# Performance work log

Hardware: AMD Instinct MI355X
Metric: run time of the kernel (lower is better)

## Reference

```python
import jax, jax.numpy as jnp
from jax import lax
import numpy as np

B, CIN, L = 16, 512, 1024
COUT, K = 1024, 5          # conv out channels (GLU halves to 512), kernel size
DW = 512                    # word_feat == attn_channels == img_conv channels
HW = 196                    # 14*14 image feature locations


def setup_inputs() -> dict:
    key = jax.random.key(0)
    ks = jax.random.split(key, 8)
    s = 0.02
    return {
        "x": jax.random.normal(ks[0], (B, CIN, L), jnp.float32),
        "word_embed": jax.random.normal(ks[1], (B, L, DW), jnp.float32),
        "img_conv": jax.random.normal(ks[2], (B, DW, 14, 14), jnp.float32),
        "prev_attn": jnp.zeros((B, L, HW), jnp.float32),  # passed through, unused
        "conv_v": jax.random.normal(ks[3], (COUT, CIN, K), jnp.float32) * s,
        "conv_g": jnp.ones((COUT,), jnp.float32),
        "conv_b": jnp.zeros((COUT,), jnp.float32),
        "fc1_w": jax.random.normal(ks[4], (DW, DW), jnp.float32) * s,
        "fc1_b": jnp.zeros((DW,), jnp.float32),
        "fc2_w": jax.random.normal(ks[5], (DW, DW), jnp.float32) * s,
        "fc2_b": jnp.zeros((DW,), jnp.float32),
    }


def reference(x, word_embed, img_conv, prev_attn,
              conv_v, conv_g, conv_b, fc1_w, fc1_b, fc2_w, fc2_b):
    k = conv_v.shape[-1]
    # weight norm (PyTorch default dim=0): w = g * v / ||v||_{(in,k)}
    v_norm = jnp.sqrt(jnp.sum(conv_v * conv_v, axis=(1, 2), keepdims=True))
    w = (conv_g[:, None, None] / v_norm) * conv_v
    # Conv1d, padding=k-1 on both sides -> length L + k - 1 after ConvS2S trim
    y = lax.conv_general_dilated(x, w, window_strides=(1,),
                                 padding=[(k - 1, k - 1)],
                                 dimension_numbers=("NCH", "OIH", "NCH"))
    y = y + conv_b[None, :, None]
    # dropout is identity in eval mode
    a, b = jnp.split(y, 2, axis=1)          # GLU over channel dim
    h = a * jax.nn.sigmoid(b)
    h = h[:, :, : -(k - 1)]                  # [B, DW, L]
    identity_attn = h
    # attn_fc1 on [B, L, DW] then add word embeddings
    q = jnp.einsum("bcl,ac->bla", h, fc1_w) + fc1_b + word_embed  # [B, L, DW]
    feat = img_conv.reshape(img_conv.shape[0], img_conv.shape[1], -1)  # [B, DW, HW]
    score = jnp.einsum("bla,bap->blp", q, feat)   # [B, L, HW]
    attn = jax.nn.softmax(score, axis=-1)         # softmax over image locations
    ctx = jnp.einsum("blp,bap->bla", attn, feat)  # [B, L, DW]
    o = jnp.einsum("bla,ca->blc", ctx, fc2_w) + fc2_b
    out = o.transpose(0, 2, 1) + identity_attn
    # identity.shape == out.shape (input_feat == output_feat/2) -> no downsample
    out = out + x
    return (out, word_embed, img_conv, attn)
```

## Files before the change

kernel.cpp:

```cpp
#include <hip/hip_runtime.h>
#include <math.h>

#define NB   16
#define NCIN 512
#define NL   1024
#define NCOUT 1024
#define NK   5
#define NDW  512
#define NHW  196
#define NP   208
#define NPK  224
#define NLG  1028

typedef unsigned short ushort_t;
typedef unsigned int uint_t;
typedef __attribute__((ext_vector_type(8))) short bf16x8;
typedef __attribute__((ext_vector_type(4))) float f32x4;

static __device__ __forceinline__ ushort_t f2bf(float f) {
  uint_t u = __builtin_bit_cast(uint_t, f);
  u += 0x7fff + ((u >> 16) & 1);
  return (ushort_t)(u >> 16);
}
static __device__ __forceinline__ float bf2f(ushort_t u) {
  uint_t v = ((uint_t)u) << 16;
  return __builtin_bit_cast(float, v);
}

#define BARM()    asm volatile("s_barrier" ::: "memory")
#define WAITVM8() asm volatile("s_waitcnt vmcnt(8)" ::: "memory")
#define WAITVM0() asm volatile("s_waitcnt vmcnt(0)" ::: "memory")

static __device__ __forceinline__ void gld16(const ushort_t* g, ushort_t* l) {
  __builtin_amdgcn_global_load_lds(
      (const __attribute__((address_space(1))) unsigned int*)g,
      (__attribute__((address_space(3))) unsigned int*)l, 16, 0, 0);
}

__global__ __launch_bounds__(256) void wnorm_kernel(
    const float* __restrict__ v, const float* __restrict__ g,
    ushort_t* __restrict__ wperm) {
  const int o = blockIdx.x;
  const float* vr = v + (size_t)o * (NCIN * NK);
  float s = 0.f;
  for (int j = threadIdx.x; j < NCIN * NK; j += 256) {
    float t = vr[j];
    s += t * t;
  }
  for (int off = 32; off; off >>= 1) s += __shfl_down(s, off, 64);
  __shared__ float red[4];
  __shared__ float scale_s;
  const int wid = threadIdx.x >> 6;
  if ((threadIdx.x & 63) == 0) red[wid] = s;
  __syncthreads();
  if (threadIdx.x == 0) {
    float tot = red[0] + red[1] + red[2] + red[3];
    scale_s = g[o] / sqrtf(tot);
  }
  __syncthreads();
  const float scale = scale_s;
  const int isB = (o >= NDW) ? 1 : 0;
  const int c = o - isB * NDW;
  const int j = (c >> 5) * 64 + isB * 32 + (c & 31);
#pragma unroll
  for (int dk = 0; dk < NK; ++dk) {
    for (int ci = threadIdx.x; ci < NCIN; ci += 256) {
      wperm[((size_t)dk * NCOUT + j) * NCIN + ci] = f2bf(vr[ci * NK + dk] * scale);
    }
  }
}

__global__ __launch_bounds__(256) void xpose_kernel(
    const float* __restrict__ x, ushort_t* __restrict__ xT) {
  const int b = blockIdx.z;
  const int ci0 = blockIdx.y * 64;
  const int l0 = blockIdx.x * 64;
  const int tid = threadIdx.x;
  __shared__ float t[64][65];
  const float* xb = x + ((size_t)b * NCIN + ci0) * NL + l0;
#pragma unroll
  for (int r = 0; r < 4; ++r) {
    int row = r * 16 + (tid >> 4);
    int col = (tid & 15) * 4;
    float4 v = *(const float4*)&xb[(size_t)row * NL + col];
    t[row][col + 0] = v.x; t[row][col + 1] = v.y;
    t[row][col + 2] = v.z; t[row][col + 3] = v.w;
  }
  __syncthreads();
  ushort_t* xo = xT + ((size_t)b * NLG + l0 + 4) * NCIN + ci0;
#pragma unroll
  for (int r = 0; r < 4; ++r) {
    int lrow = r * 16 + (tid >> 4);
    int cic = (tid & 15) * 4;
    ushort4 o4;
    o4.x = f2bf(t[cic + 0][lrow]);
    o4.y = f2bf(t[cic + 1][lrow]);
    o4.z = f2bf(t[cic + 2][lrow]);
    o4.w = f2bf(t[cic + 3][lrow]);
    *(ushort4*)&xo[(size_t)lrow * NCIN + cic] = o4;
  }
  if (blockIdx.x == 0) {
    for (int i = tid; i < 4 * 64; i += 256) {
      int rr = i >> 6, cc = i & 63;
      xT[((size_t)b * NLG + rr) * NCIN + ci0 + cc] = 0;
    }
  }
}

__global__ __launch_bounds__(256) void wcvt_kernel(
    const float* __restrict__ w1, const float* __restrict__ w2,
    ushort_t* __restrict__ w1bf, ushort_t* __restrict__ w2bf) {
  const int i = (blockIdx.x * 256 + threadIdx.x) * 4;
  {
    float4 v = *(const float4*)&w1[i];
    ushort4 o; o.x = f2bf(v.x); o.y = f2bf(v.y); o.z = f2bf(v.z); o.w = f2bf(v.w);
    *(ushort4*)&w1bf[i] = o;
  }
  {
    float4 v = *(const float4*)&w2[i];
    ushort4 o; o.x = f2bf(v.x); o.y = f2bf(v.y); o.z = f2bf(v.z); o.w = f2bf(v.w);
    *(ushort4*)&w2bf[i] = o;
  }
}

__global__ __launch_bounds__(256) void ftrans_kernel(
    const float* __restrict__ feat, ushort_t* __restrict__ fThi,
    ushort_t* __restrict__ fTlo, ushort_t* __restrict__ fbf) {
  const int b = blockIdx.y;
  const int a0 = blockIdx.x * 64;
  const int tid = threadIdx.x;
  __shared__ float t[64][200];

  const float* fb_ = feat + ((size_t)b * NDW + a0) * NHW;
#pragma unroll
  for (int pp = 0; pp < 16; ++pp) {
    int row = pp * 4 + (tid >> 6);
#pragma unroll
    for (int cc = 0; cc < 4; ++cc) {
      int col = cc * 64 + (tid & 63);
      if (col < NHW) t[row][col] = fb_[(size_t)row * NHW + col];
    }
  }
  __syncthreads();

  for (int pp = 0; pp < 13; ++pp) {
    int p = pp * 16 + (tid >> 4);
    int j = (tid & 15) * 4;
    ushort4 hi4, lo4;
#pragma unroll
    for (int k = 0; k < 4; ++k) {
      float v = (p < NHW) ? t[j + k][p] : 0.f;
      ushort_t h = f2bf(v);
      float lof = v - bf2f(h);
      ushort_t l = f2bf(lof);
      ((ushort_t*)&hi4)[k] = h;
      ((ushort_t*)&lo4)[k] = l;
    }
    size_t base = ((size_t)b * NP + p) * NDW + a0 + j;
    *(ushort4*)&fThi[base] = hi4;
    *(ushort4*)&fTlo[base] = lo4;
  }

#pragma unroll
  for (int cc = 0; cc < 4; ++cc) {
    int col = cc * 64 + (tid & 63);
    if (col < NPK) {
#pragma unroll
      for (int rr = 0; rr < 16; ++rr) {
        int al = rr * 4 + (tid >> 6);
        float v = (col < NHW) ? t[al][col] : 0.f;
        fbf[((size_t)b * NDW + a0 + al) * NPK + col] = f2bf(v);
      }
    }
  }
}

__global__ __launch_bounds__(512, 2) void conv_glu_mfma(
    const ushort_t* __restrict__ xT, const ushort_t* __restrict__ wperm,
    const float* __restrict__ conv_b, ushort_t* __restrict__ hbfT) {
  const int bb = blockIdx.x >> 2;
  const int l0 = (blockIdx.x & 3) * 256;
  const int by = blockIdx.y;
  const int tid = threadIdx.x;
  const int wid = tid >> 6;
  const int lane = tid & 63;
  const int wm = wid >> 2;
  const int wn = wid & 3;
  const int quad = lane >> 4;
  const int l16 = lane & 15;
  const int sw = (l16 & 7) << 3;
  const int csrc = ((lane & 7) ^ (lane >> 3)) << 3;

  __shared__ ushort_t sA[2][256][64];
  __shared__ ushort_t sB[2][256][64];

  f32x4 acc[8][4];
#pragma unroll
  for (int mt = 0; mt < 8; ++mt)
#pragma unroll
    for (int nt = 0; nt < 4; ++nt) acc[mt][nt] = (f32x4){0.f, 0.f, 0.f, 0.f};

  const ushort_t* gAbase = xT + (size_t)(bb * NLG + l0) * NCIN;
  const int r0 = wid * 8 + (lane >> 3);
  ushort_t* lA0 = &sA[0][0][0] + (wid * 64 + lane) * 8;
  ushort_t* lB0 = &sB[0][0][0] + (wid * 64 + lane) * 8;

  auto stage = [&](int tt, int s) {
    const int dk = tt >> 3;
    const int ci0 = (tt & 7) << 6;
    const ushort_t* gA = gAbase + (size_t)dk * NCIN + ci0 + csrc;
    const ushort_t* gB = wperm + ((size_t)dk * NCOUT + by * 256) * NCIN + ci0 + csrc;
    ushort_t* lA = lA0 + s * (256 * 64);
    ushort_t* lB = lB0 + s * (256 * 64);
#pragma unroll
    for (int c = 0; c < 4; ++c) {
      gld16(gA + (size_t)(r0 + c * 64) * NCIN, lA + c * 4096);
      gld16(gB + (size_t)(r0 + c * 64) * NCIN, lB + c * 4096);
    }
  };

  stage(0, 0);
  stage(1, 1);
  WAITVM8();
  BARM();

  for (int t = 0; t < 40; ++t) {
    const int s = t & 1;
    bf16x8 af[4][2], bfr[4][2];

#pragma unroll
    for (int mt = 0; mt < 4; ++mt)
#pragma unroll
      for (int ks = 0; ks < 2; ++ks)
        af[mt][ks] = *(const bf16x8*)&sA[s][wm * 128 + mt * 16 + l16]
                                        [(ks * 32 + quad * 8) ^ sw];
#pragma unroll
    for (int nt = 0; nt < 2; ++nt)
#pragma unroll
      for (int ks = 0; ks < 2; ++ks)
        bfr[nt][ks] = *(const bf16x8*)&sB[s][wn * 64 + nt * 16 + l16]
                                         [(ks * 32 + quad * 8) ^ sw];
    BARM();
    __builtin_amdgcn_s_setprio(1);
#pragma unroll
    for (int ks = 0; ks < 2; ++ks)
#pragma unroll
      for (int nt = 0; nt < 2; ++nt)
#pragma unroll
        for (int mt = 0; mt < 4; ++mt)
          acc[mt][nt] = __builtin_amdgcn_mfma_f32_16x16x32_bf16(
              af[mt][ks], bfr[nt][ks], acc[mt][nt], 0, 0, 0);
    __builtin_amdgcn_s_setprio(0);
    BARM();

#pragma unroll
    for (int nt = 2; nt < 4; ++nt)
#pragma unroll
      for (int ks = 0; ks < 2; ++ks)
        bfr[nt][ks] = *(const bf16x8*)&sB[s][wn * 64 + nt * 16 + l16]
                                         [(ks * 32 + quad * 8) ^ sw];
    BARM();
    __builtin_amdgcn_s_setprio(1);
#pragma unroll
    for (int ks = 0; ks < 2; ++ks)
#pragma unroll
      for (int nt = 2; nt < 4; ++nt)
#pragma unroll
        for (int mt = 0; mt < 4; ++mt)
          acc[mt][nt] = __builtin_amdgcn_mfma_f32_16x16x32_bf16(
              af[mt][ks], bfr[nt][ks], acc[mt][nt], 0, 0, 0);
    __builtin_amdgcn_s_setprio(0);
    BARM();

#pragma unroll
    for (int mt = 0; mt < 4; ++mt)
#pragma unroll
      for (int ks = 0; ks < 2; ++ks)
        af[mt][ks] = *(const bf16x8*)&sA[s][wm * 128 + (4 + mt) * 16 + l16]
                                        [(ks * 32 + quad * 8) ^ sw];
    BARM();
    __builtin_amdgcn_s_setprio(1);
#pragma unroll
    for (int ks = 0; ks < 2; ++ks)
#pragma unroll
      for (int nt = 0; nt < 2; ++nt)
#pragma unroll
        for (int mt = 0; mt < 4; ++mt)
          acc[4 + mt][nt] = __builtin_amdgcn_mfma_f32_16x16x32_bf16(
              af[mt][ks], bfr[nt][ks], acc[4 + mt][nt], 0, 0, 0);
    __builtin_amdgcn_s_setprio(0);
    BARM();

    if (t < 38) stage(t + 2, s);
    __builtin_amdgcn_s_setprio(1);
#pragma unroll
    for (int ks = 0; ks < 2; ++ks)
#pragma unroll
      for (int nt = 2; nt < 4; ++nt)
#pragma unroll
        for (int mt = 0; mt < 4; ++mt)
          acc[4 + mt][nt] = __builtin_amdgcn_mfma_f32_16x16x32_bf16(
              af[mt][ks], bfr[nt][ks], acc[4 + mt][nt], 0, 0, 0);
    __builtin_amdgcn_s_setprio(0);

    if (t < 39) {
      if (t < 38) { WAITVM8(); } else { WAITVM0(); }
      BARM();
    }
  }

#pragma unroll
  for (int nt = 0; nt < 2; ++nt) {
    const int c = by * 128 + wn * 32 + nt * 16 + l16;
    const float ba = conv_b[c];
    const float bg = conv_b[c + NDW];
#pragma unroll
    for (int mt = 0; mt < 8; ++mt) {
      const int lg = l0 + wm * 128 + mt * 16 + quad * 4;
      ushort_t* ho = hbfT + ((size_t)bb * NL + lg) * NDW + c;
#pragma unroll
      for (int r = 0; r < 4; ++r) {
        float aa = acc[mt][nt][r] + ba;
        float gg = acc[mt][nt + 2][r] + bg;
        float hv = aa * (1.f / (1.f + __expf(-gg)));
        ho[(size_t)r * NDW] = f2bf(hv);
      }
    }
  }
}

__global__ __launch_bounds__(256, 1) void attn_fused(
    const ushort_t* __restrict__ hbfT, const ushort_t* __restrict__ w1bf,
    const float* __restrict__ fb1, const float* __restrict__ we,
    const ushort_t* __restrict__ fThi, const ushort_t* __restrict__ fTlo,
    const ushort_t* __restrict__ fbf, float* __restrict__ out_attn,
    ushort_t* __restrict__ ctx_bf) {
  const int b  = blockIdx.y;
  const int l0 = blockIdx.x * 64;
  const int tid = threadIdx.x;
  const int wid = tid >> 6;
  const int lane = tid & 63;
  const int quad = lane >> 4;
  const int l16 = lane & 15;

  __shared__ ushort_t smem[69504];
  ushort_t* hT = smem;
  ushort_t* wS = smem + 33280;
  ushort_t* qh = smem + 49920;
  ushort_t* ql = smem + 52224;
  ushort_t* fh = smem + 54528;
  ushort_t* fl = smem + 62016;
  ushort_t* pa = smem;
  ushort_t* fb = smem + 14848;

#pragma unroll
  for (int it = 0; it < 16; ++it) {
    int lin = tid + it * 256;
    int r = lin >> 6, seg = lin & 63;
    *(uint4*)&hT[r * 520 + seg * 8] =
        *(const uint4*)(hbfT + ((size_t)b * NL + l0 + r) * NDW + seg * 8);
  }

  f32x4 acc[13];
#pragma unroll
  for (int nt = 0; nt < 13; ++nt) acc[nt] = (f32x4){0.f, 0.f, 0.f, 0.f};

  for (int kc = 0; kc < 16; ++kc) {
    const int a0 = kc * 32;
    __syncthreads();
    {
      int r = tid >> 2, seg = tid & 3;
#pragma unroll
      for (int it = 0; it < 4; ++it) {
        int row = it * 64 + r;
        if (row < NP) {
          size_t fsrc = ((size_t)b * NP + row) * NDW + a0 + seg * 8;
          *(uint4*)&fh[row * 36 + seg * 8] = *(const uint4*)(fThi + fsrc);
          *(uint4*)&fl[row * 36 + seg * 8] = *(const uint4*)(fTlo + fsrc);
        }
      }
#pragma unroll
      for (int it = 0; it < 8; ++it) {
        int lin = tid + it * 256;
        int rr = lin >> 6, ss = lin & 63;
        *(uint4*)&wS[rr * 520 + ss * 8] =
            *(const uint4*)(w1bf + (size_t)(a0 + rr) * NDW + ss * 8);
      }
    }
    __syncthreads();

    f32x4 aq[2][2];
    aq[0][0] = aq[0][1] = aq[1][0] = aq[1][1] = (f32x4){0.f, 0.f, 0.f, 0.f};
#pragma unroll
    for (int cs = 0; cs < 16; ++cs) {
      bf16x8 af = *(const bf16x8*)&hT[(wid * 16 + l16) * 520 + cs * 32 + quad * 8];
#pragma unroll
      for (int nt = 0; nt < 2; ++nt) {
        bf16x8 bw = *(const bf16x8*)&wS[(nt * 16 + l16) * 520 + cs * 32 + quad * 8];
        aq[cs & 1][nt] = __builtin_amdgcn_mfma_f32_16x16x32_bf16(af, bw, aq[cs & 1][nt], 0, 0, 0);
      }
    }
#pragma unroll
    for (int nt = 0; nt < 2; ++nt) {
      const int a = a0 + nt * 16 + l16;
      const float bias = fb1[a];
#pragma unroll
      for (int r = 0; r < 4; ++r) {
        const int l = l0 + wid * 16 + quad * 4 + r;
        float qv = aq[0][nt][r] + aq[1][nt][r] + bias + we[((size_t)b * NL + l) * NDW + a];
        ushort_t h = f2bf(qv);
        const int row = wid * 16 + quad * 4 + r;
        qh[row * 36 + nt * 16 + l16] = h;
        ql[row * 36 + nt * 16 + l16] = f2bf(qv - bf2f(h));
      }
    }
    __syncthreads();

    bf16x8 ah = *(const bf16x8*)&qh[(wid * 16 + l16) * 36 + quad * 8];
    bf16x8 al = *(const bf16x8*)&ql[(wid * 16 + l16) * 36 + quad * 8];
#pragma unroll
    for (int nt = 0; nt < 13; ++nt) {
      bf16x8 bh = *(const bf16x8*)&fh[(nt * 16 + l16) * 36 + quad * 8];
      bf16x8 bl = *(const bf16x8*)&fl[(nt * 16 + l16) * 36 + quad * 8];
      acc[nt] = __builtin_amdgcn_mfma_f32_16x16x32_bf16(ah, bh, acc[nt], 0, 0, 0);
      acc[nt] = __builtin_amdgcn_mfma_f32_16x16x32_bf16(al, bh, acc[nt], 0, 0, 0);
      acc[nt] = __builtin_amdgcn_mfma_f32_16x16x32_bf16(ah, bl, acc[nt], 0, 0, 0);
    }
  }

  const bool v12 = (l16 < 4);
#pragma unroll
  for (int r = 0; r < 4; ++r) {
    float mx = -1e30f;
#pragma unroll
    for (int nt = 0; nt < 12; ++nt) mx = fmaxf(mx, acc[nt][r]);
    if (v12) mx = fmaxf(mx, acc[12][r]);
#pragma unroll
    for (int off = 1; off < 16; off <<= 1) mx = fmaxf(mx, __shfl_xor(mx, off, 16));
    float ex[13];
    float sum = 0.f;
#pragma unroll
    for (int nt = 0; nt < 12; ++nt) { ex[nt] = __expf(acc[nt][r] - mx); sum += ex[nt]; }
    ex[12] = v12 ? __expf(acc[12][r] - mx) : 0.f;
    sum += ex[12];
#pragma unroll
    for (int off = 1; off < 16; off <<= 1) sum += __shfl_xor(sum, off, 16);
    const float inv = 1.f / sum;
    const int l = l0 + wid * 16 + quad * 4 + r;
    float* ao = out_attn + ((size_t)b * NL + l) * NHW;
#pragma unroll
    for (int nt = 0; nt < 13; ++nt) {
      float av = ex[nt] * inv;
      acc[nt][r] = av;
      int p = nt * 16 + l16;
      if (p < NHW) ao[p] = av;
    }
  }

  __syncthreads();

#pragma unroll
  for (int r = 0; r < 4; ++r) {
    const int row = wid * 16 + quad * 4 + r;
#pragma unroll
    for (int nt = 0; nt < 13; ++nt) {
      int p = nt * 16 + l16;
      pa[row * 232 + p] = (p < NHW) ? f2bf(acc[nt][r]) : (ushort_t)0;
    }
    pa[row * 232 + 208 + l16] = 0;
  }

  for (int ac = 0; ac < 8; ++ac) {
    const int a0 = ac * 64;
    __syncthreads();
#pragma unroll
    for (int it = 0; it < 7; ++it) {
      int lin = tid + it * 256;
      int rr = lin / 28, ss = lin % 28;
      *(uint4*)&fb[rr * 232 + ss * 8] =
          *(const uint4*)(fbf + ((size_t)b * NDW + a0 + rr) * NPK + ss * 8);
    }
    __syncthreads();
    f32x4 ca[4];
#pragma unroll
    for (int nt = 0; nt < 4; ++nt) ca[nt] = (f32x4){0.f, 0.f, 0.f, 0.f};
#pragma unroll
    for (int ks = 0; ks < 7; ++ks) {
      bf16x8 af = *(const bf16x8*)&pa[(wid * 16 + l16) * 232 + ks * 32 + quad * 8];
#pragma unroll
      for (int nt = 0; nt < 4; ++nt) {
        bf16x8 bv = *(const bf16x8*)&fb[(nt * 16 + l16) * 232 + ks * 32 + quad * 8];
        ca[nt] = __builtin_amdgcn_mfma_f32_16x16x32_bf16(af, bv, ca[nt], 0, 0, 0);
      }
    }
#pragma unroll
    for (int nt = 0; nt < 4; ++nt) {
      const int a = a0 + nt * 16 + l16;
#pragma unroll
      for (int r = 0; r < 4; ++r) {
        const int l = l0 + wid * 16 + quad * 4 + r;
        ctx_bf[((size_t)b * NL + l) * NDW + a] = f2bf(ca[nt][r]);
      }
    }
  }
}

__global__ __launch_bounds__(256, 2) void fc2_mfma(
    const ushort_t* __restrict__ w2bf, const ushort_t* __restrict__ ctx_bf,
    const float* __restrict__ fb2, const ushort_t* __restrict__ hbfT,
    const float* __restrict__ x, float* __restrict__ out0) {
  const int b  = blockIdx.z;
  const int c0 = blockIdx.y * 128;
  const int l0 = blockIdx.x * 128;
  const int tid = threadIdx.x;
  const int wid = tid >> 6;
  const int lane = tid & 63;
  const int wl = wid & 1;
  const int wc = wid >> 1;
  const int quad = lane >> 4;
  const int l16 = lane & 15;

  __shared__ ushort_t la[128][72];
  __shared__ ushort_t lb[128][72];

  f32x4 acc[4][4];
#pragma unroll
  for (int mt = 0; mt < 4; ++mt)
#pragma unroll
    for (int nt = 0; nt < 4; ++nt) acc[mt][nt] = (f32x4){0.f, 0.f, 0.f, 0.f};

  for (int a0 = 0; a0 < NDW; a0 += 64) {
    __syncthreads();
#pragma unroll
    for (int it = 0; it < 4; ++it) {
      int t = tid + it * 256;
      int r = t >> 3, seg = t & 7;
      *(uint4*)&la[r][seg * 8] = *(const uint4*)(w2bf + (size_t)(c0 + r) * NDW + a0 + seg * 8);
    }
#pragma unroll
    for (int it = 0; it < 4; ++it) {
      int t = tid + it * 256;
      int r = t >> 3, seg = t & 7;
      *(uint4*)&lb[r][seg * 8] =
          *(const uint4*)(ctx_bf + ((size_t)b * NL + l0 + r) * NDW + a0 + seg * 8);
    }
    __syncthreads();
#pragma unroll
    for (int ks = 0; ks < 2; ++ks) {
      bf16x8 af[4];
#pragma unroll
      for (int mt = 0; mt < 4; ++mt)
        af[mt] = *(const bf16x8*)&la[wl * 64 + mt * 16 + l16][ks * 32 + quad * 8];
#pragma unroll
      for (int nt = 0; nt < 4; ++nt) {
        bf16x8 bf = *(const bf16x8*)&lb[wc * 64 + nt * 16 + l16][ks * 32 + quad * 8];
#pragma unroll
        for (int mt = 0; mt < 4; ++mt)
          acc[mt][nt] = __builtin_amdgcn_mfma_f32_16x16x32_bf16(af[mt], bf, acc[mt][nt], 0, 0, 0);
      }
    }
  }

#pragma unroll
  for (int mt = 0; mt < 4; ++mt) {
    const int cb = c0 + wl * 64 + mt * 16 + quad * 4;
    float4 bias4 = *(const float4*)&fb2[cb];
#pragma unroll
    for (int nt = 0; nt < 4; ++nt) {
      const int l = l0 + wc * 64 + nt * 16 + l16;
      ushort4 h4 = *(const ushort4*)&hbfT[((size_t)b * NL + l) * NDW + cb];
      const float bias[4] = {bias4.x, bias4.y, bias4.z, bias4.w};
      const ushort_t hs[4] = {h4.x, h4.y, h4.z, h4.w};
#pragma unroll
      for (int r = 0; r < 4; ++r) {
        size_t idx = ((size_t)b * NDW + cb + r) * NL + l;
        out0[idx] = acc[mt][nt][r] + bias[r] + bf2f(hs[r]) + x[idx];
      }
    }
  }
}

extern "C" void kernel_launch(void* const* d_in, const int* in_sizes, int n_in,
                              void* d_out, int out_size, void* d_ws, size_t ws_size,
                              hipStream_t stream) {
  const float* x      = (const float*)d_in[0];
  const float* we     = (const float*)d_in[1];
  const float* img    = (const float*)d_in[2];
  const float* conv_v = (const float*)d_in[4];
  const float* conv_g = (const float*)d_in[5];
  const float* conv_b = (const float*)d_in[6];
  const float* fc1_w  = (const float*)d_in[7];
  const float* fc1_b  = (const float*)d_in[8];
  const float* fc2_w  = (const float*)d_in[9];
  const float* fc2_b  = (const float*)d_in[10];

  float* out0     = (float*)d_out;
  float* out_we   = out0 + 8388608;
  float* out_img  = out_we + 8388608;
  float* out_attn = out_img + 1605632;

  ushort_t* wsu = (ushort_t*)d_ws;
  ushort_t* wperm = wsu;
  ushort_t* xT    = wsu + 2621440;
  ushort_t* ctx_b = wsu;
  ushort_t* hbfT  = wsu + 16777216;
  ushort_t* w1bf  = wsu + 25165824;
  ushort_t* w2bf  = wsu + 25165824 + 262144;
  ushort_t* fThi  = wsu + 25690112;
  ushort_t* fTlo  = wsu + 27394048;
  ushort_t* fbf   = wsu + 29097984;

  wnorm_kernel<<<dim3(NCOUT), 256, 0, stream>>>(conv_v, conv_g, wperm);
  xpose_kernel<<<dim3(16, 8, NB), 256, 0, stream>>>(x, xT);
  wcvt_kernel<<<dim3(256), 256, 0, stream>>>(fc1_w, fc2_w, w1bf, w2bf);
  ftrans_kernel<<<dim3(8, NB), 256, 0, stream>>>(img, fThi, fTlo, fbf);

  conv_glu_mfma<<<dim3(64, 4), 512, 0, stream>>>(xT, wperm, conv_b, hbfT);
  attn_fused<<<dim3(16, NB), 256, 0, stream>>>(hbfT, w1bf, fc1_b, we,
                                               fThi, fTlo, fbf, out_attn, ctx_b);
  fc2_mfma<<<dim3(8, 4, NB), 256, 0, stream>>>(w2bf, ctx_b, fc2_b, hbfT, x, out0);

  hipMemcpyAsync(out_we, we, (size_t)8388608 * sizeof(float),
                 hipMemcpyDeviceToDevice, stream);
  hipMemcpyAsync(out_img, img, (size_t)1605632 * sizeof(float),
                 hipMemcpyDeviceToDevice, stream);
}
```

Before: 440.9 us.

## Keep attention A-operand in registers to halve LDS and allow two blocks per CU

The attention kernel now loads each wave's h rows straight into registers instead of staging the full 64x512 tile in shared memory. This cuts LDS from about 139KB to about 72KB, so the launch bound is raised to allow two blocks per CU. The word-embedding and bias loads are hoisted ahead of the sync so their latency overlaps the staging work. Separately, an lgkmcnt wait is added before a barrier in the conv GEMM loop. The cost is many more VGPRs (16 uint4 per thread), which under the 2-block bound could cause spilling.

Measured after the change: 435.5 us. No clear change (-1.2%).

```diff
diff --git a/kernel.cpp b/kernel.cpp
--- a/kernel.cpp
+++ b/kernel.cpp
@@ -27,9 +27,10 @@
   return __builtin_bit_cast(float, v);
 }
 
-#define BARM()    asm volatile("s_barrier" ::: "memory")
-#define WAITVM8() asm volatile("s_waitcnt vmcnt(8)" ::: "memory")
-#define WAITVM0() asm volatile("s_waitcnt vmcnt(0)" ::: "memory")
+#define BARM()     asm volatile("s_barrier" ::: "memory")
+#define WAITVM8()  asm volatile("s_waitcnt vmcnt(8)" ::: "memory")
+#define WAITVM0()  asm volatile("s_waitcnt vmcnt(0)" ::: "memory")
+#define WAITLGKM0() asm volatile("s_waitcnt lgkmcnt(0)" ::: "memory")
 
 static __device__ __forceinline__ void gld16(const ushort_t* g, ushort_t* l) {
   __builtin_amdgcn_global_load_lds(
@@ -289,6 +290,7 @@
           acc[4 + mt][nt] = __builtin_amdgcn_mfma_f32_16x16x32_bf16(
               af[mt][ks], bfr[nt][ks], acc[4 + mt][nt], 0, 0, 0);
     __builtin_amdgcn_s_setprio(0);
+    WAITLGKM0();
     BARM();
 
     if (t < 38) stage(t + 2, s);
@@ -329,7 +331,7 @@
   }
 }
 
-__global__ __launch_bounds__(256, 1) void attn_fused(
+__global__ __launch_bounds__(256, 2) void attn_fused(
     const ushort_t* __restrict__ hbfT, const ushort_t* __restrict__ w1bf,
     const float* __restrict__ fb1, const float* __restrict__ we,
     const ushort_t* __restrict__ fThi, const ushort_t* __restrict__ fTlo,
@@ -343,22 +345,22 @@
   const int quad = lane >> 4;
   const int l16 = lane & 15;
 
-  __shared__ ushort_t smem[69504];
-  ushort_t* hT = smem;
-  ushort_t* wS = smem + 33280;
-  ushort_t* qh = smem + 49920;
-  ushort_t* ql = smem + 52224;
-  ushort_t* fh = smem + 54528;
-  ushort_t* fl = smem + 62016;
+  __shared__ ushort_t smem[36224];
+  ushort_t* wS = smem;
+  ushort_t* fh = smem + 16640;
+  ushort_t* fl = smem + 24128;
+  ushort_t* qh = smem + 31616;
+  ushort_t* ql = smem + 33920;
   ushort_t* pa = smem;
   ushort_t* fb = smem + 14848;
 
-#pragma unroll
-  for (int it = 0; it < 16; ++it) {
-    int lin = tid + it * 256;
-    int r = lin >> 6, seg = lin & 63;
-    *(uint4*)&hT[r * 520 + seg * 8] =
-        *(const uint4*)(hbfT + ((size_t)b * NL + l0 + r) * NDW + seg * 8);
+  uint4 hreg[16];
+  {
+    const ushort_t* hrow =
+        hbfT + ((size_t)b * NL + l0 + wid * 16 + l16) * NDW + quad * 8;
+#pragma unroll
+    for (int cs = 0; cs < 16; ++cs)
+      hreg[cs] = *(const uint4*)(hrow + cs * 32);
   }
 
   f32x4 acc[13];
@@ -367,6 +369,20 @@
 
   for (int kc = 0; kc < 16; ++kc) {
     const int a0 = kc * 32;
+
+    float wev[2][4];
+    float bias[2];
+#pragma unroll
+    for (int nt = 0; nt < 2; ++nt) {
+      const int a = a0 + nt * 16 + l16;
+      bias[nt] = fb1[a];
+#pragma unroll
+      for (int r = 0; r < 4; ++r) {
+        const int l = l0 + wid * 16 + quad * 4 + r;
+        wev[nt][r] = we[((size_t)b * NL + l) * NDW + a];
+      }
+    }
+
     __syncthreads();
     {
       int r = tid >> 2, seg = tid & 3;
@@ -393,7 +409,7 @@
     aq[0][0] = aq[0][1] = aq[1][0] = aq[1][1] = (f32x4){0.f, 0.f, 0.f, 0.f};
 #pragma unroll
     for (int cs = 0; cs < 16; ++cs) {
-      bf16x8 af = *(const bf16x8*)&hT[(wid * 16 + l16) * 520 + cs * 32 + quad * 8];
+      bf16x8 af = __builtin_bit_cast(bf16x8, hreg[cs]);
 #pragma unroll
       for (int nt = 0; nt < 2; ++nt) {
         bf16x8 bw = *(const bf16x8*)&wS[(nt * 16 + l16) * 520 + cs * 32 + quad * 8];
@@ -402,12 +418,9 @@
     }
 #pragma unroll
     for (int nt = 0; nt < 2; ++nt) {
-      const int a = a0 + nt * 16 + l16;
-      const float bias = fb1[a];
 #pragma unroll
       for (int r = 0; r < 4; ++r) {
-        const int l = l0 + wid * 16 + quad * 4 + r;
-        float qv = aq[0][nt][r] + aq[1][nt][r] + bias + we[((size_t)b * NL + l) * NDW + a];
+        float qv = aq[0][nt][r] + aq[1][nt][r] + bias[nt] + wev[nt][r];
         ushort_t h = f2bf(qv);
         const int row = wid * 16 + quad * 4 + r;
         qh[row * 36 + nt * 16 + l16] = h;
```
